# Performance work log

Measured on AMD Instinct MI355X. Metric: run time of the kernel, lower is better.

Reference implementation:

```python
import jax, jax.numpy as jnp
import numpy as np

ALPHA = 0.25
GAMMA = 2.0
MARGIN = 1.0
LAMBDA_GRAPH = 0.1
N = 8192
D = 128


def setup_inputs() -> dict:
    key = jax.random.key(0)
    k1, k2, k3, k4 = jax.random.split(key, 4)
    preds = jax.random.normal(k1, (N,), dtype=jnp.float32)
    targets = jax.random.randint(k2, (N,), 0, 2).astype(jnp.float32)  # binary labels
    features = jax.random.normal(k3, (N, D), dtype=jnp.float32)
    graph_features = jax.random.normal(k4, (N, D), dtype=jnp.float32)
    return {"preds": preds, "targets": targets, "features": features,
            "graph_features": graph_features}


def _focal_loss(preds, targets):
    # numerically stable BCE-with-logits, reduction='none'
    bce = jnp.maximum(preds, 0.0) - preds * targets + jnp.log1p(jnp.exp(-jnp.abs(preds)))
    pt = jnp.exp(-bce)
    return jnp.mean(ALPHA * (1.0 - pt) ** GAMMA * bce)


def _contrastive_loss(features, labels):
    # squared pairwise distances via ||a||^2 + ||b||^2 - 2 a.b  -> [N, N]
    sqn = jnp.sum(features * features, axis=-1)
    sq = sqn[:, None] + sqn[None, :] - 2.0 * (features @ features.T)
    sq = jnp.maximum(sq, 0.0)
    # safe sqrt (gradient-safe at 0)
    pos = sq > 0.0
    dist = jnp.where(pos, jnp.sqrt(jnp.where(pos, sq, 1.0)), 0.0)
    same = labels[:, None] == labels[None, :]
    # same-label pairs: dist^2 == sq ; different: clamp(margin - dist, 0)^2
    per_pair = jnp.where(same, sq, jnp.maximum(MARGIN - dist, 0.0) ** 2)
    return jnp.mean(per_pair)  # sum / N^2


def _graph_reg_loss(graph_features):
    diff = graph_features[1:] - graph_features[:-1]
    return jnp.mean(jnp.sqrt(jnp.sum(diff * diff, axis=1)))


def reference(preds, targets, features, graph_features):
    return (_focal_loss(preds, targets)
            + _contrastive_loss(features, targets)
            + LAMBDA_GRAPH * _graph_reg_loss(graph_features))
```

## Files before the change

kernel.cpp:

```cpp
#include <hip/hip_runtime.h>
#include <hip/hip_bf16.h>


#define N_PTS 8192
#define DIM 128

typedef __bf16 bf16x8 __attribute__((ext_vector_type(8)));
typedef float f32x4 __attribute__((ext_vector_type(4)));

#define NPAIR 2080
#define NPREP 128
#define NFOCAL 32
#define NGRAPH 256
#define NMAIN (NPAIR + NPREP + NFOCAL + NGRAPH)

#define VPART_OFF 0
#define SPART_OFF 131072
#define CPART_OFF 133120
#define FPART_OFF 166400
#define GPART_OFF 166912

#define LDS_BYTES (8192 + 8192 + 1024 + 1024)
__device__ __forceinline__ int uoff(int g, int q, int m) {
    return ((g * 4 + q) * 16 + m) * 16;
}

__device__ __forceinline__ float ssq4(const float4 a) {
    return a.x * a.x + a.y * a.y + a.z * a.z + a.w * a.w;
}
__device__ __forceinline__ void store8(void* dst, float4 a, float4 b, float sc) {
    union { __bf16 h[8]; uint4 u; } p;
    p.h[0] = (__bf16)(sc * a.x); p.h[1] = (__bf16)(sc * a.y);
    p.h[2] = (__bf16)(sc * a.z); p.h[3] = (__bf16)(sc * a.w);
    p.h[4] = (__bf16)(sc * b.x); p.h[5] = (__bf16)(sc * b.y);
    p.h[6] = (__bf16)(sc * b.z); p.h[7] = (__bf16)(sc * b.w);
    *reinterpret_cast<uint4*>(dst) = p.u;
}
__device__ __forceinline__ void store4(void* dst, float4 a, float sc) {
    union { __bf16 h[4]; uint2 u; } p;
    p.h[0] = (__bf16)(sc * a.x); p.h[1] = (__bf16)(sc * a.y);
    p.h[2] = (__bf16)(sc * a.z); p.h[3] = (__bf16)(sc * a.w);
    *reinterpret_cast<uint2*>(dst) = p.u;
}
__device__ __forceinline__ bf16x8 pack8(const float4 a, const float4 b) {
    bf16x8 r;
    r[0] = (__bf16)a.x; r[1] = (__bf16)a.y; r[2] = (__bf16)a.z; r[3] = (__bf16)a.w;
    r[4] = (__bf16)b.x; r[5] = (__bf16)b.y; r[6] = (__bf16)b.z; r[7] = (__bf16)b.w;
    return r;
}

template<bool DIAG>
__device__ __forceinline__ float scan_slow(const f32x4 (&acc)[4][4],
                                           const f32x4 (&sqni)[4], const f32x4 (&ti4)[4],
                                           const float (&sqnj)[4], const float (&tj4)[4],
                                           int wm, int wn, int quad, int m15) {
    float lsum = 0.f;
    #pragma unroll
    for (int tm = 0; tm < 4; ++tm) {
        #pragma unroll
        for (int tn = 0; tn < 4; ++tn) {
            const int jl = wn * 64 + tn * 16 + m15;
            #pragma unroll
            for (int e = 0; e < 4; ++e) {
                const float sq = sqni[tm][e] + sqnj[tn] - 2.f * acc[tm][tn][e];
                bool excl = (ti4[tm][e] == tj4[tn]);
                if (DIAG) {
                    const int il = wm * 64 + tm * 16 + quad * 4 + e;
                    excl = excl || (jl <= il);
                }
                if (!excl && sq < 1.f) {
                    const float d = sqrtf(fmaxf(sq, 0.f));
                    const float m = 1.f - d;
                    lsum += 2.f * m * m;
                }
            }
        }
    }
    return lsum;
}

__global__ __launch_bounds__(256, 4) void main_kernel(const float* __restrict__ feat,
                                                      const float* __restrict__ preds,
                                                      const float* __restrict__ targets,
                                                      const float* __restrict__ gfeat,
                                                      float* __restrict__ vpart,
                                                      float* __restrict__ spart,
                                                      float* __restrict__ c_part,
                                                      float* __restrict__ f_part,
                                                      float* __restrict__ g_part) {
    __shared__ __align__(16) char smem[LDS_BYTES];
    const int bx = blockIdx.x;
    const int tid = threadIdx.x;
    const int w = tid >> 6, lane = tid & 63;

    if (bx < NPAIR) {
        const int u = bx;
        const int vv = 2079 - u;
        int k = (int)((sqrtf(8.f * (float)vv + 1.f) - 1.f) * 0.5f);
        while ((k + 1) * (k + 2) / 2 <= vv) ++k;
        while (k * (k + 1) / 2 > vv) --k;
        const int bi = 63 - k;
        const int bj = 63 - (vv - k * (k + 1) / 2);

        const int quad = lane >> 4, m15 = lane & 15;
        const int wm = w >> 1, wn = w & 1;

        char* Ap = smem;
        char* Bp = smem + 8192;
        float* s24A = reinterpret_cast<float*>(smem + 16384);
        float* s24B = reinterpret_cast<float*>(smem + 17408);

        {
            const int r = tid >> 1, h = tid & 1;
            const int g = r >> 4, m = r & 15;
            const float4* f4 = reinterpret_cast<const float4*>(feat);
            const int ab = (bi * 128 + r) * 32 + h * 3;
            const int bb = (bj * 128 + r) * 32 + h * 3;
            const float4 a0 = f4[ab], a1 = f4[ab + 1], a2 = f4[ab + 2];
            const float4 b0 = f4[bb], b1 = f4[bb + 1], b2 = f4[bb + 2];
            s24A[r * 2 + h] = ssq4(a0) + ssq4(a1) + ssq4(a2);
            s24B[r * 2 + h] = ssq4(b0) + ssq4(b1) + ssq4(b2);
            if (h == 0) {
                store8(Ap + uoff(g, 0, m), a0, a1, -2.f);
                store4(Ap + uoff(g, 1, m), a2, -2.f);
                store8(Bp + uoff(g, 0, m), b0, b1, 1.f);
                store4(Bp + uoff(g, 1, m), b2, 1.f);
            } else {
                store4(Ap + uoff(g, 1, m) + 8, a0, -2.f);
                store8(Ap + uoff(g, 2, m), a1, a2, -2.f);
                store4(Bp + uoff(g, 1, m) + 8, b0, 1.f);
                store8(Bp + uoff(g, 2, m), b1, b2, 1.f);
            }
            __syncthreads();
            if (tid < 128) {
                const int rr = tid, gg = rr >> 4, mm = rr & 15;
                const float sqa = s24A[rr * 2] + s24A[rr * 2 + 1];
                const float sqb = s24B[rr * 2] + s24B[rr * 2 + 1];
                union { __bf16 x[8]; uint4 u; } ua, ub;
                #pragma unroll
                for (int i = 0; i < 8; ++i) { ua.x[i] = (__bf16)0.f; ub.x[i] = (__bf16)0.f; }
                ua.x[0] = (__bf16)sqa; ua.x[1] = (__bf16)1.f;
                ub.x[0] = (__bf16)1.f; ub.x[1] = (__bf16)sqb;
                *reinterpret_cast<uint4*>(Ap + uoff(gg, 3, mm)) = ua.u;
                *reinterpret_cast<uint4*>(Bp + uoff(gg, 3, mm)) = ub.u;
            }
            __syncthreads();
        }

        bf16x8 afs[4], bfs[4];
        #pragma unroll
        for (int t = 0; t < 4; ++t) {
            afs[t] = *reinterpret_cast<const bf16x8*>(Ap + uoff(wm * 4 + t, quad, m15));
            bfs[t] = *reinterpret_cast<const bf16x8*>(Bp + uoff(wn * 4 + t, quad, m15));
        }
        f32x4 acc[4][4];
        #pragma unroll
        for (int a = 0; a < 4; ++a)
            #pragma unroll
            for (int b = 0; b < 4; ++b) acc[a][b] = (f32x4){0.f, 0.f, 0.f, 0.f};
        #pragma unroll
        for (int tm = 0; tm < 4; ++tm)
            #pragma unroll
            for (int tn = 0; tn < 4; ++tn)
                acc[tm][tn] = __builtin_amdgcn_mfma_f32_16x16x32_bf16(
                    afs[tm], bfs[tn], acc[tm][tn], 0, 0, 0);

        float minv = 1e30f;
        #pragma unroll
        for (int tm = 0; tm < 4; ++tm)
            #pragma unroll
            for (int tn = 0; tn < 4; ++tn)
                #pragma unroll
                for (int e = 0; e < 4; ++e)
                    minv = fminf(minv, acc[tm][tn][e]);

        float lsum = 0.f;
        if (__any(minv < 2.f)) {
            const int ibase = bi * 128 + wm * 64, jbase = bj * 128 + wn * 64;
            float qi = 0.f, qj = 0.f;
            {
                const float4* ri = reinterpret_cast<const float4*>(feat + (ibase + lane) * DIM);
                const float4* rj = reinterpret_cast<const float4*>(feat + (jbase + lane) * DIM);
                #pragma unroll 8
                for (int c2 = 0; c2 < 32; ++c2) {
                    const float4 x = ri[c2]; qi += x.x * x.x + x.y * x.y + x.z * x.z + x.w * x.w;
                    const float4 y = rj[c2]; qj += y.x * y.x + y.y * y.y + y.z * y.z + y.w * y.w;
                }
            }
            f32x4 sqni[4], ti4[4];
            float sqnj[4], tj4[4];
            #pragma unroll
            for (int tm = 0; tm < 4; ++tm) {
                #pragma unroll
                for (int e = 0; e < 4; ++e) sqni[tm][e] = __shfl(qi, tm * 16 + quad * 4 + e);
                ti4[tm] = *reinterpret_cast<const f32x4*>(targets + ibase + tm * 16 + quad * 4);
            }
            #pragma unroll
            for (int tn = 0; tn < 4; ++tn) {
                sqnj[tn] = __shfl(qj, tn * 16 + m15);
                tj4[tn] = targets[jbase + tn * 16 + m15];
            }
            #pragma unroll
            for (int a = 0; a < 4; ++a)
                #pragma unroll
                for (int b = 0; b < 4; ++b) acc[a][b] = (f32x4){0.f, 0.f, 0.f, 0.f};
            for (int ks = 0; ks < 4; ++ks) {
                bf16x8 af2[4], bf2[4];
                #pragma unroll
                for (int t = 0; t < 4; ++t) {
                    const float* pa = feat + (ibase + t * 16 + m15) * DIM + 8 * (quad + 4 * ks);
                    af2[t] = pack8(*reinterpret_cast<const float4*>(pa),
                                   *reinterpret_cast<const float4*>(pa + 4));
                    const float* pb = feat + (jbase + t * 16 + m15) * DIM + 8 * (quad + 4 * ks);
                    bf2[t] = pack8(*reinterpret_cast<const float4*>(pb),
                                   *reinterpret_cast<const float4*>(pb + 4));
                }
                #pragma unroll
                for (int tm = 0; tm < 4; ++tm)
                    #pragma unroll
                    for (int tn = 0; tn < 4; ++tn)
                        acc[tm][tn] = __builtin_amdgcn_mfma_f32_16x16x32_bf16(
                            af2[tm], bf2[tn], acc[tm][tn], 0, 0, 0);
            }
            lsum = (bi == bj)
                ? scan_slow<true >(acc, sqni, ti4, sqnj, tj4, wm, wn, quad, m15)
                : scan_slow<false>(acc, sqni, ti4, sqnj, tj4, wm, wn, quad, m15);
            #pragma unroll
            for (int off = 32; off > 0; off >>= 1) lsum += __shfl_down(lsum, off);
        }
        if (lane == 0) c_part[u * 4 + w] = lsum;
    } else if (bx < NPAIR + NPREP) {
        const int b = bx - NPAIR;
        float* fA = reinterpret_cast<float*>(smem);
        float* f1 = reinterpret_cast<float*>(smem + 2048);
        float (*sred)[3] = reinterpret_cast<float(*)[3]>(smem + 4096);
        const float2* feat2 = reinterpret_cast<const float2*>(feat);
        float2 accA = {0.f, 0.f}, acc1 = {0.f, 0.f};
        float ssqA = 0.f, ssq1 = 0.f, n1 = 0.f;
        int r = b * 64 + w * 16;
        #pragma unroll 4
        for (int i = 0; i < 16; ++i, ++r) {
            const float2 v = feat2[r * 64 + lane];
            const float tr = targets[r];
            accA.x += v.x; accA.y += v.y;
            acc1.x += tr * v.x; acc1.y += tr * v.y;
            const float s2 = v.x * v.x + v.y * v.y;
            ssqA += s2; ssq1 += tr * s2; n1 += tr;
        }
        fA[w * 128 + 2 * lane] = accA.x; fA[w * 128 + 2 * lane + 1] = accA.y;
        f1[w * 128 + 2 * lane] = acc1.x; f1[w * 128 + 2 * lane + 1] = acc1.y;
        #pragma unroll
        for (int off = 32; off > 0; off >>= 1) {
            ssqA += __shfl_down(ssqA, off);
            ssq1 += __shfl_down(ssq1, off);
        }
        if (lane == 0) { sred[w][0] = ssqA; sred[w][1] = ssq1; sred[w][2] = n1; }
        __syncthreads();
        if (tid < 128) {
            const int d = tid;
            const float c1 = f1[d] + f1[128 + d] + f1[256 + d] + f1[384 + d];
            const float ca = fA[d] + fA[128 + d] + fA[256 + d] + fA[384 + d];
            vpart[b * 256 + tid] = ca - c1;
        } else {
            const int d = tid - 128;
            vpart[b * 256 + tid] = f1[d] + f1[128 + d] + f1[256 + d] + f1[384 + d];
        }
        if (tid == 0) {
            float4 s;
            s.x = sred[0][0] + sred[1][0] + sred[2][0] + sred[3][0];
            s.y = sred[0][1] + sred[1][1] + sred[2][1] + sred[3][1];
            s.z = sred[0][2] + sred[1][2] + sred[2][2] + sred[3][2];
            s.w = 0.f;
            *reinterpret_cast<float4*>(spart + b * 4) = s;
        }
    } else if (bx < NPAIR + NPREP + NFOCAL) {
        const int b = bx - NPAIR - NPREP;
        const int i = b * 256 + tid;
        const float p = preds[i], t = targets[i];
        const float bce = fmaxf(p, 0.f) - p * t + log1pf(expf(-fabsf(p)));
        const float pt = expf(-bce);
        const float om = 1.f - pt;
        float fv = 0.25f * om * om * bce;
        #pragma unroll
        for (int off = 32; off > 0; off >>= 1) fv += __shfl_down(fv, off);
        if (lane == 0) f_part[b * 4 + w] = fv;
    } else {
        const int b = bx - NPAIR - NPREP - NFOCAL;
        float ga = 0.f;
        #pragma unroll
        for (int it = 0; it < 8; ++it) {
            const int r = b * 4 + w + it * 1024;
            if (r < N_PTS - 1) {
                const float2 a = *reinterpret_cast<const float2*>(gfeat + r * DIM + lane * 2);
                const float2 bb = *reinterpret_cast<const float2*>(gfeat + (r + 1) * DIM + lane * 2);
                const float dx = bb.x - a.x, dy = bb.y - a.y;
                float s = dx * dx + dy * dy;
                #pragma unroll
                for (int off = 32; off > 0; off >>= 1) s += __shfl_down(s, off);
                if (lane == 0) ga += sqrtf(s);
            }
        }
        if (lane == 0) g_part[b * 4 + w] = ga;
    }
}

__global__ __launch_bounds__(256) void finalize_kernel(const float* __restrict__ c_part,
                                                       const float* __restrict__ f_part,
                                                       const float* __restrict__ g_part,
                                                       const float* __restrict__ vpart,
                                                       const float* __restrict__ spart,
                                                       float* __restrict__ out) {
    __shared__ double sC[4], sF[4], sG[4], sV[4], sST[4], sS1[4], sN1[4];
    const int tid = threadIdx.x;
    const int w = tid >> 6, lane = tid & 63;

    double c = 0.0;
    for (int i = tid; i < NPAIR * 4; i += 256) c += (double)c_part[i];
    double f = (tid < NFOCAL * 4) ? (double)f_part[tid] : 0.0;
    double g = 0.0;
    for (int i = tid; i < NGRAPH * 4; i += 256) g += (double)g_part[i];

    float V = 0.f;
    #pragma unroll 8
    for (int b2 = 0; b2 < 128; ++b2) V += vpart[b2 * 256 + tid];
    double vsq = (double)V * (double)V;

    double st = 0.0, s1 = 0.0, n1 = 0.0;
    if (tid < 128) {
        const float4 s = *reinterpret_cast<const float4*>(spart + tid * 4);
        st = s.x; s1 = s.y; n1 = s.z;
    }
    #pragma unroll
    for (int off = 32; off > 0; off >>= 1) {
        c += __shfl_down(c, off);
        f += __shfl_down(f, off);
        g += __shfl_down(g, off);
        vsq += __shfl_down(vsq, off);
        st += __shfl_down(st, off);
        s1 += __shfl_down(s1, off);
        n1 += __shfl_down(n1, off);
    }
    if (lane == 0) {
        sC[w] = c; sF[w] = f; sG[w] = g; sV[w] = vsq;
        sST[w] = st; sS1[w] = s1; sN1[w] = n1;
    }
    __syncthreads();
    if (tid == 0) {
        const double cs = sC[0] + sC[1] + sC[2] + sC[3];
        const double fs = sF[0] + sF[1] + sF[2] + sF[3];
        const double gs = sG[0] + sG[1] + sG[2] + sG[3];
        const double v0sq = sV[0] + sV[1];
        const double v1sq = sV[2] + sV[3];
        const double stot = sST[0] + sST[1] + sST[2] + sST[3];
        const double s1s  = sS1[0] + sS1[1] + sS1[2] + sS1[3];
        const double n1s  = sN1[0] + sN1[1] + sN1[2] + sN1[3];
        const double n0s = (double)N_PTS - n1s;
        const double s0s = stot - s1s;
        const double same = 2.0 * (n0s * s0s - v0sq) + 2.0 * (n1s * s1s - v1sq);
        out[0] = (float)((cs + same) / ((double)N_PTS * (double)N_PTS)
                         + fs / (double)N_PTS
                         + 0.1 * (gs / (double)(N_PTS - 1)));
    }
}

extern "C" void kernel_launch(void* const* d_in, const int* in_sizes, int n_in,
                              void* d_out, int out_size, void* d_ws, size_t ws_size,
                              hipStream_t stream) {
    const float* preds    = (const float*)d_in[0];
    const float* targets  = (const float*)d_in[1];
    const float* features = (const float*)d_in[2];
    const float* gfeat    = (const float*)d_in[3];
    char* ws = (char*)d_ws;
    float* vpart  = (float*)(ws + VPART_OFF);
    float* spart  = (float*)(ws + SPART_OFF);
    float* c_part = (float*)(ws + CPART_OFF);
    float* f_part = (float*)(ws + FPART_OFF);
    float* g_part = (float*)(ws + GPART_OFF);
    float* out = (float*)d_out;

    main_kernel<<<NMAIN, 256, 0, stream>>>(features, preds, targets, gfeat,
                                           vpart, spart, c_part, f_part, g_part);
    finalize_kernel<<<1, 256, 0, stream>>>(c_part, f_part, g_part, vpart, spart, out);
}
```

Before: 107.9 us.

## Use 1024-thread blocks covering 256x256 super-tiles of pairwise distances

Main kernel blocks grow from 256 to 1024 threads. Each pair block now stages a 256-row super-tile of A and B into LDS and four 4-wave groups compute 128x128 sub-tiles. Sub-tiles below the diagonal in diagonal super-blocks are masked off. This reduces the block count and shares staged features across four sub-tiles, but it wastes a quarter of the work on diagonal super-blocks, uses more LDS and may lower occupancy. The auxiliary blocks (prep, focal, graph) are remapped to process four chunks each.

Result: no change. 107.6 us (-0.2%).

```diff
diff --git a/kernel.cpp b/kernel.cpp
--- a/kernel.cpp
+++ b/kernel.cpp
@@ -8,21 +8,21 @@
 typedef __bf16 bf16x8 __attribute__((ext_vector_type(8)));
 typedef float f32x4 __attribute__((ext_vector_type(4)));
 
-#define NPAIR 2080
-#define NPREP 128
-#define NFOCAL 32
-#define NGRAPH 256
-#define NMAIN (NPAIR + NPREP + NFOCAL + NGRAPH)
+#define NPAIRB 528
+#define NPREPB 32
+#define NFOCALB 8
+#define NGRAPHB 64
+#define NMAIN (NPAIRB + NPREPB + NFOCALB + NGRAPHB)
 
 #define VPART_OFF 0
 #define SPART_OFF 131072
 #define CPART_OFF 133120
-#define FPART_OFF 166400
-#define GPART_OFF 166912
-
-#define LDS_BYTES (8192 + 8192 + 1024 + 1024)
-__device__ __forceinline__ int uoff(int g, int q, int m) {
-    return ((g * 4 + q) * 16 + m) * 16;
+#define FPART_OFF 166912
+#define GPART_OFF 167424
+
+#define LDS_BYTES 36864
+__device__ __forceinline__ int uoff(int g, int qd, int m) {
+    return ((g * 4 + qd) * 16 + m) * 16;
 }
 
 __device__ __forceinline__ float ssq4(const float4 a) {
@@ -53,7 +53,7 @@
 __device__ __forceinline__ float scan_slow(const f32x4 (&acc)[4][4],
                                            const f32x4 (&sqni)[4], const f32x4 (&ti4)[4],
                                            const float (&sqnj)[4], const float (&tj4)[4],
-                                           int wm, int wn, int quad, int m15) {
+                                           int wm, int wn, int qd, int m15) {
     float lsum = 0.f;
     #pragma unroll
     for (int tm = 0; tm < 4; ++tm) {
@@ -65,7 +65,7 @@
                 const float sq = sqni[tm][e] + sqnj[tn] - 2.f * acc[tm][tn][e];
                 bool excl = (ti4[tm][e] == tj4[tn]);
                 if (DIAG) {
-                    const int il = wm * 64 + tm * 16 + quad * 4 + e;
+                    const int il = wm * 64 + tm * 16 + qd * 4 + e;
                     excl = excl || (jl <= il);
                 }
                 if (!excl && sq < 1.f) {
@@ -79,79 +79,81 @@
     return lsum;
 }
 
-__global__ __launch_bounds__(256, 4) void main_kernel(const float* __restrict__ feat,
-                                                      const float* __restrict__ preds,
-                                                      const float* __restrict__ targets,
-                                                      const float* __restrict__ gfeat,
-                                                      float* __restrict__ vpart,
-                                                      float* __restrict__ spart,
-                                                      float* __restrict__ c_part,
-                                                      float* __restrict__ f_part,
-                                                      float* __restrict__ g_part) {
+__global__ __launch_bounds__(1024, 4) void main_kernel(const float* __restrict__ feat,
+                                                       const float* __restrict__ preds,
+                                                       const float* __restrict__ targets,
+                                                       const float* __restrict__ gfeat,
+                                                       float* __restrict__ vpart,
+                                                       float* __restrict__ spart,
+                                                       float* __restrict__ c_part,
+                                                       float* __restrict__ f_part,
+                                                       float* __restrict__ g_part) {
     __shared__ __align__(16) char smem[LDS_BYTES];
     const int bx = blockIdx.x;
     const int tid = threadIdx.x;
     const int w = tid >> 6, lane = tid & 63;
 
-    if (bx < NPAIR) {
+    if (bx < NPAIRB) {
         const int u = bx;
-        const int vv = 2079 - u;
+        const int vv = 527 - u;
         int k = (int)((sqrtf(8.f * (float)vv + 1.f) - 1.f) * 0.5f);
         while ((k + 1) * (k + 2) / 2 <= vv) ++k;
         while (k * (k + 1) / 2 > vv) --k;
-        const int bi = 63 - k;
-        const int bj = 63 - (vv - k * (k + 1) / 2);
-
-        const int quad = lane >> 4, m15 = lane & 15;
-        const int wm = w >> 1, wn = w & 1;
+        const int sbi = 31 - k;
+        const int sbj = 31 - (vv - k * (k + 1) / 2);
 
         char* Ap = smem;
-        char* Bp = smem + 8192;
-        float* s24A = reinterpret_cast<float*>(smem + 16384);
-        float* s24B = reinterpret_cast<float*>(smem + 17408);
+        char* Bp = smem + 16384;
+        float* s24A = reinterpret_cast<float*>(smem + 32768);
+        float* s24B = reinterpret_cast<float*>(smem + 34816);
 
         {
             const int r = tid >> 1, h = tid & 1;
-            const int g = r >> 4, m = r & 15;
+            const bool isA = r < 256;
+            const int rr = isA ? r : r - 256;
+            const int grow = (isA ? sbi : sbj) * 256 + rr;
             const float4* f4 = reinterpret_cast<const float4*>(feat);
-            const int ab = (bi * 128 + r) * 32 + h * 3;
-            const int bb = (bj * 128 + r) * 32 + h * 3;
-            const float4 a0 = f4[ab], a1 = f4[ab + 1], a2 = f4[ab + 2];
-            const float4 b0 = f4[bb], b1 = f4[bb + 1], b2 = f4[bb + 2];
-            s24A[r * 2 + h] = ssq4(a0) + ssq4(a1) + ssq4(a2);
-            s24B[r * 2 + h] = ssq4(b0) + ssq4(b1) + ssq4(b2);
+            const int o = grow * 32 + h * 3;
+            const float4 a0 = f4[o], a1 = f4[o + 1], a2 = f4[o + 2];
+            const int g = rr >> 4, m = rr & 15;
+            char* P = isA ? Ap : Bp;
+            const float sc = isA ? -2.f : 1.f;
+            (isA ? s24A : s24B)[rr * 2 + h] = ssq4(a0) + ssq4(a1) + ssq4(a2);
             if (h == 0) {
-                store8(Ap + uoff(g, 0, m), a0, a1, -2.f);
-                store4(Ap + uoff(g, 1, m), a2, -2.f);
-                store8(Bp + uoff(g, 0, m), b0, b1, 1.f);
-                store4(Bp + uoff(g, 1, m), b2, 1.f);
+                store8(P + uoff(g, 0, m), a0, a1, sc);
+                store4(P + uoff(g, 1, m), a2, sc);
             } else {
-                store4(Ap + uoff(g, 1, m) + 8, a0, -2.f);
-                store8(Ap + uoff(g, 2, m), a1, a2, -2.f);
-                store4(Bp + uoff(g, 1, m) + 8, b0, 1.f);
-                store8(Bp + uoff(g, 2, m), b1, b2, 1.f);
+                store4(P + uoff(g, 1, m) + 8, a0, sc);
+                store8(P + uoff(g, 2, m), a1, a2, sc);
             }
             __syncthreads();
-            if (tid < 128) {
-                const int rr = tid, gg = rr >> 4, mm = rr & 15;
-                const float sqa = s24A[rr * 2] + s24A[rr * 2 + 1];
-                const float sqb = s24B[rr * 2] + s24B[rr * 2 + 1];
-                union { __bf16 x[8]; uint4 u; } ua, ub;
-                #pragma unroll
-                for (int i = 0; i < 8; ++i) { ua.x[i] = (__bf16)0.f; ub.x[i] = (__bf16)0.f; }
+            if (tid < 256) {
+                const int gg = tid >> 4, mm = tid & 15;
+                const float sqa = s24A[tid * 2] + s24A[tid * 2 + 1];
+                const float sqb = s24B[tid * 2] + s24B[tid * 2 + 1];
+                union { __bf16 x[8]; uint4 uu; } ua, ub;
+                #pragma unroll
+                for (int i2 = 0; i2 < 8; ++i2) { ua.x[i2] = (__bf16)0.f; ub.x[i2] = (__bf16)0.f; }
                 ua.x[0] = (__bf16)sqa; ua.x[1] = (__bf16)1.f;
                 ub.x[0] = (__bf16)1.f; ub.x[1] = (__bf16)sqb;
-                *reinterpret_cast<uint4*>(Ap + uoff(gg, 3, mm)) = ua.u;
-                *reinterpret_cast<uint4*>(Bp + uoff(gg, 3, mm)) = ub.u;
+                *reinterpret_cast<uint4*>(Ap + uoff(gg, 3, mm)) = ua.uu;
+                *reinterpret_cast<uint4*>(Bp + uoff(gg, 3, mm)) = ub.uu;
             }
             __syncthreads();
         }
 
+        const int qd = lane >> 4, m15 = lane & 15;
+        const int q = w >> 2, wq = w & 3;
+        const int qm = q >> 1, qn = q & 1;
+        const int BI = sbi * 2 + qm, BJ = sbj * 2 + qn;
+        const int wm = wq >> 1, wn = wq & 1;
+        const bool active = (BI <= BJ);
+
         bf16x8 afs[4], bfs[4];
         #pragma unroll
         for (int t = 0; t < 4; ++t) {
-            afs[t] = *reinterpret_cast<const bf16x8*>(Ap + uoff(wm * 4 + t, quad, m15));
-            bfs[t] = *reinterpret_cast<const bf16x8*>(Bp + uoff(wn * 4 + t, quad, m15));
+            afs[t] = *reinterpret_cast<const bf16x8*>(Ap + uoff(qm * 8 + wm * 4 + t, qd, m15));
+            bfs[t] = *reinterpret_cast<const bf16x8*>(Bp + uoff(qn * 8 + wn * 4 + t, qd, m15));
         }
         f32x4 acc[4][4];
         #pragma unroll
@@ -173,10 +175,11 @@
                 #pragma unroll
                 for (int e = 0; e < 4; ++e)
                     minv = fminf(minv, acc[tm][tn][e]);
+        if (!active) minv = 1e30f;
 
         float lsum = 0.f;
         if (__any(minv < 2.f)) {
-            const int ibase = bi * 128 + wm * 64, jbase = bj * 128 + wn * 64;
+            const int ibase = BI * 128 + wm * 64, jbase = BJ * 128 + wn * 64;
             float qi = 0.f, qj = 0.f;
             {
                 const float4* ri = reinterpret_cast<const float4*>(feat + (ibase + lane) * DIM);
@@ -192,8 +195,8 @@
             #pragma unroll
             for (int tm = 0; tm < 4; ++tm) {
                 #pragma unroll
-                for (int e = 0; e < 4; ++e) sqni[tm][e] = __shfl(qi, tm * 16 + quad * 4 + e);
-                ti4[tm] = *reinterpret_cast<const f32x4*>(targets + ibase + tm * 16 + quad * 4);
+                for (int e = 0; e < 4; ++e) sqni[tm][e] = __shfl(qi, tm * 16 + qd * 4 + e);
+                ti4[tm] = *reinterpret_cast<const f32x4*>(targets + ibase + tm * 16 + qd * 4);
             }
             #pragma unroll
             for (int tn = 0; tn < 4; ++tn) {
@@ -208,10 +211,10 @@
                 bf16x8 af2[4], bf2[4];
                 #pragma unroll
                 for (int t = 0; t < 4; ++t) {
-                    const float* pa = feat + (ibase + t * 16 + m15) * DIM + 8 * (quad + 4 * ks);
+                    const float* pa = feat + (ibase + t * 16 + m15) * DIM + 8 * (qd + 4 * ks);
                     af2[t] = pack8(*reinterpret_cast<const float4*>(pa),
                                    *reinterpret_cast<const float4*>(pa + 4));
-                    const float* pb = feat + (jbase + t * 16 + m15) * DIM + 8 * (quad + 4 * ks);
+                    const float* pb = feat + (jbase + t * 16 + m15) * DIM + 8 * (qd + 4 * ks);
                     bf2[t] = pack8(*reinterpret_cast<const float4*>(pb),
                                    *reinterpret_cast<const float4*>(pb + 4));
                 }
@@ -222,22 +225,24 @@
                         acc[tm][tn] = __builtin_amdgcn_mfma_f32_16x16x32_bf16(
                             af2[tm], bf2[tn], acc[tm][tn], 0, 0, 0);
             }
-            lsum = (bi == bj)
-                ? scan_slow<true >(acc, sqni, ti4, sqnj, tj4, wm, wn, quad, m15)
-                : scan_slow<false>(acc, sqni, ti4, sqnj, tj4, wm, wn, quad, m15);
+            lsum = (BI == BJ)
+                ? scan_slow<true >(acc, sqni, ti4, sqnj, tj4, wm, wn, qd, m15)
+                : scan_slow<false>(acc, sqni, ti4, sqnj, tj4, wm, wn, qd, m15);
             #pragma unroll
             for (int off = 32; off > 0; off >>= 1) lsum += __shfl_down(lsum, off);
         }
-        if (lane == 0) c_part[u * 4 + w] = lsum;
-    } else if (bx < NPAIR + NPREP) {
-        const int b = bx - NPAIR;
-        float* fA = reinterpret_cast<float*>(smem);
-        float* f1 = reinterpret_cast<float*>(smem + 2048);
-        float (*sred)[3] = reinterpret_cast<float(*)[3]>(smem + 4096);
+        if (lane == 0) c_part[u * 16 + w] = lsum;
+    } else if (bx < NPAIRB + NPREPB) {
+        const int cq = tid >> 8, t256 = tid & 255;
+        const int w4 = (tid >> 6) & 3;
+        const int chunk = (bx - NPAIRB) * 4 + cq;
+        float* fA = reinterpret_cast<float*>(smem) + cq * 1024;
+        float* f1 = fA + 512;
+        float* sred = reinterpret_cast<float*>(smem + 16384);
         const float2* feat2 = reinterpret_cast<const float2*>(feat);
         float2 accA = {0.f, 0.f}, acc1 = {0.f, 0.f};
         float ssqA = 0.f, ssq1 = 0.f, n1 = 0.f;
-        int r = b * 64 + w * 16;
+        int r = chunk * 64 + w4 * 16;
         #pragma unroll 4
         for (int i = 0; i < 16; ++i, ++r) {
             const float2 v = feat2[r * 64 + lane];
@@ -247,35 +252,41 @@
             const float s2 = v.x * v.x + v.y * v.y;
             ssqA += s2; ssq1 += tr * s2; n1 += tr;
         }
-        fA[w * 128 + 2 * lane] = accA.x; fA[w * 128 + 2 * lane + 1] = accA.y;
-        f1[w * 128 + 2 * lane] = acc1.x; f1[w * 128 + 2 * lane + 1] = acc1.y;
+        fA[w4 * 128 + 2 * lane] = accA.x; fA[w4 * 128 + 2 * lane + 1] = accA.y;
+        f1[w4 * 128 + 2 * lane] = acc1.x; f1[w4 * 128 + 2 * lane + 1] = acc1.y;
         #pragma unroll
         for (int off = 32; off > 0; off >>= 1) {
             ssqA += __shfl_down(ssqA, off);
             ssq1 += __shfl_down(ssq1, off);
         }
-        if (lane == 0) { sred[w][0] = ssqA; sred[w][1] = ssq1; sred[w][2] = n1; }
+        if (lane == 0) {
+            sred[(cq * 4 + w4) * 3 + 0] = ssqA;
+            sred[(cq * 4 + w4) * 3 + 1] = ssq1;
+            sred[(cq * 4 + w4) * 3 + 2] = n1;
+        }
         __syncthreads();
-        if (tid < 128) {
-            const int d = tid;
+        if (t256 < 128) {
+            const int d = t256;
             const float c1 = f1[d] + f1[128 + d] + f1[256 + d] + f1[384 + d];
             const float ca = fA[d] + fA[128 + d] + fA[256 + d] + fA[384 + d];
-            vpart[b * 256 + tid] = ca - c1;
+            vpart[chunk * 256 + t256] = ca - c1;
         } else {
-            const int d = tid - 128;
-            vpart[b * 256 + tid] = f1[d] + f1[128 + d] + f1[256 + d] + f1[384 + d];
-        }
-        if (tid == 0) {
+            const int d = t256 - 128;
+            vpart[chunk * 256 + t256] = f1[d] + f1[128 + d] + f1[256 + d] + f1[384 + d];
+        }
+        if (t256 == 0) {
             float4 s;
-            s.x = sred[0][0] + sred[1][0] + sred[2][0] + sred[3][0];
-            s.y = sred[0][1] + sred[1][1] + sred[2][1] + sred[3][1];
-            s.z = sred[0][2] + sred[1][2] + sred[2][2] + sred[3][2];
+            s.x = sred[cq * 12 + 0] + sred[cq * 12 + 3] + sred[cq * 12 + 6] + sred[cq * 12 + 9];
+            s.y = sred[cq * 12 + 1] + sred[cq * 12 + 4] + sred[cq * 12 + 7] + sred[cq * 12 + 10];
+            s.z = sred[cq * 12 + 2] + sred[cq * 12 + 5] + sred[cq * 12 + 8] + sred[cq * 12 + 11];
             s.w = 0.f;
-            *reinterpret_cast<float4*>(spart + b * 4) = s;
-        }
-    } else if (bx < NPAIR + NPREP + NFOCAL) {
-        const int b = bx - NPAIR - NPREP;
-        const int i = b * 256 + tid;
+            *reinterpret_cast<float4*>(spart + chunk * 4) = s;
+        }
+    } else if (bx < NPAIRB + NPREPB + NFOCALB) {
+        const int cq = tid >> 8, t256 = tid & 255;
+        const int w4 = (tid >> 6) & 3;
+        const int chunk = (bx - NPAIRB - NPREPB) * 4 + cq;
+        const int i = chunk * 256 + t256;
         const float p = preds[i], t = targets[i];
         const float bce = fmaxf(p, 0.f) - p * t + log1pf(expf(-fabsf(p)));
         const float pt = expf(-bce);
@@ -283,13 +294,15 @@
         float fv = 0.25f * om * om * bce;
         #pragma unroll
         for (int off = 32; off > 0; off >>= 1) fv += __shfl_down(fv, off);
-        if (lane == 0) f_part[b * 4 + w] = fv;
+        if (lane == 0) f_part[chunk * 4 + w4] = fv;
     } else {
-        const int b = bx - NPAIR - NPREP - NFOCAL;
+        const int cq = tid >> 8;
+        const int w4 = (tid >> 6) & 3;
+        const int chunk = (bx - NPAIRB - NPREPB - NFOCALB) * 4 + cq;
         float ga = 0.f;
         #pragma unroll
         for (int it = 0; it < 8; ++it) {
-            const int r = b * 4 + w + it * 1024;
+            const int r = chunk * 4 + w4 + it * 1024;
             if (r < N_PTS - 1) {
                 const float2 a = *reinterpret_cast<const float2*>(gfeat + r * DIM + lane * 2);
                 const float2 bb = *reinterpret_cast<const float2*>(gfeat + (r + 1) * DIM + lane * 2);
@@ -300,7 +313,7 @@
                 if (lane == 0) ga += sqrtf(s);
             }
         }
-        if (lane == 0) g_part[b * 4 + w] = ga;
+        if (lane == 0) g_part[chunk * 4 + w4] = ga;
     }
 }
 
@@ -315,10 +328,10 @@
     const int w = tid >> 6, lane = tid & 63;
 
     double c = 0.0;
-    for (int i = tid; i < NPAIR * 4; i += 256) c += (double)c_part[i];
-    double f = (tid < NFOCAL * 4) ? (double)f_part[tid] : 0.0;
+    for (int i = tid; i < NPAIRB * 16; i += 256) c += (double)c_part[i];
+    double f = (tid < 128) ? (double)f_part[tid] : 0.0;
     double g = 0.0;
-    for (int i = tid; i < NGRAPH * 4; i += 256) g += (double)g_part[i];
+    for (int i = tid; i < 1024; i += 256) g += (double)g_part[i];
 
     float V = 0.f;
     #pragma unroll 8
@@ -378,7 +391,7 @@
     float* g_part = (float*)(ws + GPART_OFF);
     float* out = (float*)d_out;
 
-    main_kernel<<<NMAIN, 256, 0, stream>>>(features, preds, targets, gfeat,
-                                           vpart, spart, c_part, f_part, g_part);
+    main_kernel<<<NMAIN, 1024, 0, stream>>>(features, preds, targets, gfeat,
+                                            vpart, spart, c_part, f_part, g_part);
     finalize_kernel<<<1, 256, 0, stream>>>(c_part, f_part, g_part, vpart, spart, out);
 }
```
